# Kernel tuning notes

Hardware: AMD Instinct MI355X
Metric: run time of the kernel (lower is better)

## Reference

```python
import jax, jax.numpy as jnp
import numpy as np

N_A = 100000   # articles
N_U = 100000   # users
E   = 1600000  # edges per edge type (avg degree 16)
D_A = 300      # article text-embedding dim
D_U = 64       # user feature dim
H   = 64       # hidden_channels
OUT = 2        # out_channels


def _lin(k, out_d, in_d, scale=0.05):
    kw, kb = jax.random.split(k)
    return (jax.random.normal(kw, (out_d, in_d)) * scale,
            jax.random.normal(kb, (out_d,)) * scale)


def setup_inputs():
    key = jax.random.key(0)
    ks = jax.random.split(key, 20)
    inp = {
        "x_article": jax.random.normal(ks[0], (N_A, D_A)),
        "x_user":    jax.random.normal(ks[1], (N_U, D_U)),
        "ei_posts":  jax.random.randint(ks[2], (2, E), 0, N_U),  # user -> article (row0 src user, row1 dst article)
        "ei_pb":     jax.random.randint(ks[3], (2, E), 0, N_A),  # article -> user
    }
    # input projections per node type
    inp["w_in_a"], inp["b_in_a"] = _lin(ks[4], H, D_A)
    inp["w_in_u"], inp["b_in_u"] = _lin(ks[5], H, D_U)
    # SAGEConv params per (layer, edge type): lin_l (with bias) on aggregated src, lin_r (no bias) on dst
    i = 6
    for layer in ("c1", "c2"):
        for et in ("p", "b"):  # p = posts (user->article), b = posted_by (article->user)
            wl, bl = _lin(ks[i], H, H); i += 1
            wr, _  = _lin(ks[i], H, H); i += 1
            inp[f"{layer}{et}_wl"] = wl
            inp[f"{layer}{et}_bl"] = bl
            inp[f"{layer}{et}_wr"] = wr
    inp["w_out"], inp["b_out"] = _lin(ks[i], OUT, H)
    return inp


def _sage(x_src, x_dst, edge_index, wl, bl, wr, n_dst):
    """PyG SAGEConv((-1,-1), H): lin_l(mean_neighbors(x_src)) + lin_r(x_dst)."""
    src, dst = edge_index[0], edge_index[1]
    msg = x_src[src]                                        # [E, H] gather
    agg = jax.ops.segment_sum(msg, dst, num_segments=n_dst)  # [n_dst, H]
    cnt = jax.ops.segment_sum(jnp.ones((edge_index.shape[1],), x_src.dtype), dst, num_segments=n_dst)
    agg = agg / jnp.maximum(cnt, 1.0)[:, None]               # mean aggregation
    return agg @ wl.T + bl + x_dst @ wr.T


def reference(x_article, x_user, ei_posts, ei_pb,
              w_in_a, b_in_a, w_in_u, b_in_u,
              c1p_wl, c1p_bl, c1p_wr, c1b_wl, c1b_bl, c1b_wr,
              c2p_wl, c2p_bl, c2p_wr, c2b_wl, c2b_bl, c2b_wr,
              w_out, b_out):
    # per-node-type input projection + ReLU
    a = jax.nn.relu(x_article @ w_in_a.T + b_in_a)  # [N_A, H]
    u = jax.nn.relu(x_user @ w_in_u.T + b_in_u)      # [N_U, H]
    # conv1 (HeteroConv mean over edge types is trivial: 1 edge type per dst type) + ReLU
    a1 = jax.nn.relu(_sage(u, a, ei_posts, c1p_wl, c1p_bl, c1p_wr, N_A))
    u1 = jax.nn.relu(_sage(a, u, ei_pb,    c1b_wl, c1b_bl, c1b_wr, N_U))
    # conv2; only the 'article' output is used by the model head
    a2 = _sage(u1, a1, ei_posts, c2p_wl, c2p_bl, c2p_wr, N_A)
    return a2 @ w_out.T + b_out  # [N_A, OUT]
```

## Files before the change

kernel.cpp:

```cpp
#include <hip/hip_runtime.h>

#define N_NODES 100000
#define EDGES   1600000
#define H 64
#define OFFPAD 100352
#define NB2 391
#define CHUNK 8192
#define NCHUNK 196
#define LOSTRIDE 392

typedef unsigned int u32;
typedef unsigned short u16;
typedef short bf16x8 __attribute__((ext_vector_type(8)));
typedef float f32x4  __attribute__((ext_vector_type(4)));

__device__ __forceinline__ void bfsplit(float x, u32& h, u32& lo) {
    union { float f; u32 u; } c; c.f = x;
    u32 hu = (c.u + 0x7fffu + ((c.u >> 16) & 1u)) & 0xffff0000u;
    h = hu >> 16;
    union { u32 u; float f; } hb; hb.u = hu;
    union { float f; u32 u; } r; r.f = x - hb.f;
    lo = (r.u + 0x7fffu + ((r.u >> 16) & 1u)) >> 16;
}
__device__ __forceinline__ u16 bfrne(float x) {
    union { float f; u32 u; } c; c.f = x;
    return (u16)((c.u + 0x7fffu + ((c.u >> 16) & 1u)) >> 16);
}
__device__ __forceinline__ float bflo(u32 w)  { union { u32 u; float f; } c; c.u = w << 16; return c.f; }
__device__ __forceinline__ float bfhi(u32 w)  { union { u32 u; float f; } c; c.u = w & 0xffff0000u; return c.f; }

__global__ __launch_bounds__(256) void prep_weights(
    const float* __restrict__ w_a, const float* __restrict__ w_u,
    const float* __restrict__ b_wl, const float* __restrict__ b_wr,
    const float* __restrict__ p_wl, const float* __restrict__ p_wr,
    u32* __restrict__ pa_h, u32* __restrict__ pa_l,
    u32* __restrict__ pu_h, u32* __restrict__ pu_l,
    u32* __restrict__ pb_h, u32* __restrict__ pb_l,
    u32* __restrict__ pp_h, u32* __restrict__ pp_l)
{
    const int t = blockIdx.x * 256 + threadIdx.x;
    float v0 = 0.f, v1 = 0.f; u32* dh; u32* dl; int idx;
    if (t < 10240) {
        const int row = t / 160, u = t - row * 160, k = 2 * u;
        if (k < 300)     v0 = w_a[row * 300 + k];
        if (k + 1 < 300) v1 = w_a[row * 300 + k + 1];
        dh = pa_h; dl = pa_l; idx = t;
    } else if (t < 12288) {
        idx = t - 10240;
        const int row = idx >> 5, u = idx & 31, k = 2 * u;
        v0 = w_u[row * 64 + k]; v1 = w_u[row * 64 + k + 1];
        dh = pu_h; dl = pu_l;
    } else if (t < 16384) {
        idx = t - 12288;
        const int row = idx >> 6, u = idx & 63, k = 2 * u;
        if (k < 64) { v0 = b_wl[row * 64 + k];      v1 = b_wl[row * 64 + k + 1]; }
        else        { v0 = b_wr[row * 64 + k - 64]; v1 = b_wr[row * 64 + k - 63]; }
        dh = pb_h; dl = pb_l;
    } else {
        idx = t - 16384;
        const int row = idx >> 6, u = idx & 63, k = 2 * u;
        if (k < 64) { v0 = p_wl[row * 64 + k];      v1 = p_wl[row * 64 + k + 1]; }
        else        { v0 = p_wr[row * 64 + k - 64]; v1 = p_wr[row * 64 + k - 63]; }
        dh = pp_h; dl = pp_l;
    }
    u32 h0, l0, h1, l1; bfsplit(v0, h0, l0); bfsplit(v1, h1, l1);
    dh[idx] = h0 | (h1 << 16);
    dl[idx] = l0 | (l1 << 16);
}

template<int D, int KPAD>
__global__ __launch_bounds__(256) void proj_mfma(
    const float* __restrict__ x,
    const u32* __restrict__ wh_g, const u32* __restrict__ wl_g,
    const float* __restrict__ b, float* __restrict__ out, u16* __restrict__ outb)
{
    constexpr int NT = KPAD / 64;
    __shared__ u32 Xh[64 * 32], Xl[64 * 32], Wh[64 * 32], Wl[64 * 32];
    const int tid  = threadIdx.x;
    const int base = blockIdx.x * 64;
    const int l  = tid & 63;
    const int wv = tid >> 6;
    const int arow = wv * 16 + (l & 15);
    const int kg = l >> 4;
    f32x4 acc[4] = {};

    for (int t = 0; t < NT; ++t) {
        const int k0 = t * 64;
        for (int i = tid; i < 1024; i += 256) {
            const int row = i >> 4, j = i & 15;
            const int k = k0 + 4 * j;
            const int u = 2 * j;
            const int widx = (row << 5) | (u ^ ((row & 7) << 2));
            const int rr = min(base + row, N_NODES - 1);
            float4 v = make_float4(0.f, 0.f, 0.f, 0.f);
            if (k + 4 <= D) {
                v = *(const float4*)&x[(size_t)rr * D + k];
            } else {
                const float* xr = &x[(size_t)rr * D];
                if (k     < D) v.x = xr[k];
                if (k + 1 < D) v.y = xr[k + 1];
                if (k + 2 < D) v.z = xr[k + 2];
                if (k + 3 < D) v.w = xr[k + 3];
            }
            u32 h0, l0, h1, l1, h2, l2, h3, l3;
            bfsplit(v.x, h0, l0); bfsplit(v.y, h1, l1);
            bfsplit(v.z, h2, l2); bfsplit(v.w, h3, l3);
            *(uint2*)&Xh[widx] = make_uint2(h0 | (h1 << 16), h2 | (h3 << 16));
            *(uint2*)&Xl[widx] = make_uint2(l0 | (l1 << 16), l2 | (l3 << 16));
            const int wo = row * (KPAD / 2) + (k0 >> 1) + u;
            *(uint2*)&Wh[widx] = *(const uint2*)&wh_g[wo];
            *(uint2*)&Wl[widx] = *(const uint2*)&wl_g[wo];
        }
        __syncthreads();
        #pragma unroll
        for (int s = 0; s < 2; ++s) {
            const int ka = (arow << 5) + ((s * 16 + kg * 4) ^ ((arow & 7) << 2));
            const bf16x8 ah = *(const bf16x8*)&Xh[ka];
            const bf16x8 al = *(const bf16x8*)&Xl[ka];
            #pragma unroll
            for (int c = 0; c < 4; ++c) {
                const int brow = c * 16 + (l & 15);
                const int kb = (brow << 5) + ((s * 16 + kg * 4) ^ ((brow & 7) << 2));
                const bf16x8 bh = *(const bf16x8*)&Wh[kb];
                const bf16x8 bl = *(const bf16x8*)&Wl[kb];
                acc[c] = __builtin_amdgcn_mfma_f32_16x16x32_bf16(ah, bh, acc[c], 0, 0, 0);
                acc[c] = __builtin_amdgcn_mfma_f32_16x16x32_bf16(ah, bl, acc[c], 0, 0, 0);
                acc[c] = __builtin_amdgcn_mfma_f32_16x16x32_bf16(al, bh, acc[c], 0, 0, 0);
            }
        }
        __syncthreads();
    }

    const int orow0 = base + wv * 16 + (l >> 4) * 4;
    #pragma unroll
    for (int c = 0; c < 4; ++c) {
        const int col = c * 16 + (l & 15);
        const float bv = b[col];
        #pragma unroll
        for (int i = 0; i < 4; ++i) {
            const int row = orow0 + i;
            if (row < N_NODES) {
                const float v = fmaxf(acc[c][i] + bv, 0.f);
                out[(size_t)row * H + col] = v;
                outb[(size_t)row * H + col] = bfrne(v);
            }
        }
    }
}

__global__ __launch_bounds__(256) void sort_fill(
    const int* __restrict__ ei_p, const int* __restrict__ ei_b,
    int* __restrict__ lo_p, int* __restrict__ lo_b,
    int* __restrict__ sz_p, int* __restrict__ sz_b,
    int* __restrict__ raw_p, int* __restrict__ raw_b)
{
    __shared__ int cnt[NB2];
    __shared__ int loc[NB2 + 1];
    int b = blockIdx.x;
    const int* __restrict__ ei; int* __restrict__ lo; int* __restrict__ sz; int* __restrict__ raw;
    if (b < NCHUNK) { ei = ei_p; lo = lo_p; sz = sz_p; raw = raw_p; }
    else { b -= NCHUNK; ei = ei_b; lo = lo_b; sz = sz_b; raw = raw_b; }
    const int tid = threadIdx.x;
    const int e0 = b * CHUNK, e1 = min(e0 + CHUNK, EDGES);

    for (int i = tid; i < NB2; i += 256) cnt[i] = 0;
    __syncthreads();
    for (int e = e0 + tid; e < e1; e += 256)
        atomicAdd(&cnt[ei[EDGES + e] >> 8], 1);
    __syncthreads();
    for (int i = tid; i < NB2; i += 256)
        if (cnt[i]) atomicAdd(&sz[i], cnt[i]);
    if (tid == 0) {
        int run = 0;
        for (int i = 0; i < NB2; ++i) { loc[i] = run; run += cnt[i]; }
        loc[NB2] = run;
    }
    __syncthreads();
    for (int i = tid; i <= NB2; i += 256) lo[b * LOSTRIDE + i] = loc[i];
    for (int i = tid; i < NB2; i += 256) cnt[i] = loc[i];
    __syncthreads();
    for (int e = e0 + tid; e < e1; e += 256) {
        const int d = ei[EDGES + e], s = ei[e];
        const int pos = atomicAdd(&cnt[d >> 8], 1);
        raw[e0 + pos] = (s << 8) | (d & 255);
    }
}

__global__ __launch_bounds__(256) void scan_boff(
    const int* __restrict__ sz_p, const int* __restrict__ sz_b,
    int* __restrict__ boff_p, int* __restrict__ boff_b,
    int* __restrict__ off_p, int* __restrict__ off_b)
{
    __shared__ int part[256];
    const int* sz = blockIdx.x ? sz_b : sz_p;
    int* boff = blockIdx.x ? boff_b : boff_p;
    int* off  = blockIdx.x ? off_b : off_p;
    const int t = threadIdx.x;
    const int i0 = 2 * t, i1 = 2 * t + 1;
    const int v0 = (i0 < NB2) ? sz[i0] : 0;
    const int v1 = (i1 < NB2) ? sz[i1] : 0;
    part[t] = v0 + v1;
    __syncthreads();
    for (int d = 1; d < 256; d <<= 1) {
        int x = (t >= d) ? part[t - d] : 0;
        __syncthreads();
        part[t] += x;
        __syncthreads();
    }
    const int excl = part[t] - (v0 + v1);
    if (i0 < NB2) boff[i0] = excl;
    if (i1 < NB2) boff[i1] = excl + v0;
    if (t == 0) { boff[NB2] = EDGES; off[N_NODES] = EDGES; }
}

__global__ __launch_bounds__(256) void bucket_sort2(
    const int* __restrict__ raw_p, const int* __restrict__ raw_b,
    const int* __restrict__ lo_p, const int* __restrict__ lo_b,
    const int* __restrict__ boff_p, const int* __restrict__ boff_b,
    int* __restrict__ off_p, int* __restrict__ off_b,
    int* __restrict__ csr_p, int* __restrict__ csr_b)
{
    __shared__ int cnt[256];
    __shared__ int cur[256];
    __shared__ int sb[NCHUNK], se[NCHUNK];
    int k = blockIdx.x;
    const int* raw; const int* lo; const int* boff; int* off; int* csr;
    if (k < NB2) { raw = raw_p; lo = lo_p; boff = boff_p; off = off_p; csr = csr_p; }
    else { k -= NB2; raw = raw_b; lo = lo_b; boff = boff_b; off = off_b; csr = csr_b; }
    const int tid = threadIdx.x;
    cnt[tid] = 0;
    if (tid < NCHUNK) {
        sb[tid] = lo[tid * LOSTRIDE + k];
        se[tid] = lo[tid * LOSTRIDE + k + 1];
    }
    __syncthreads();
    if (tid < NCHUNK) {
        const int base = tid * CHUNK;
        for (int e = sb[tid]; e < se[tid]; ++e)
            atomicAdd(&cnt[raw[base + e] & 255], 1);
    }
    __syncthreads();
    if (tid == 0) {
        int run = boff[k];
        for (int i = 0; i < 256; ++i) { cur[i] = run; run += cnt[i]; }
    }
    __syncthreads();
    {
        const int node = (k << 8) + tid;
        if (node < N_NODES) off[node] = cur[tid];
    }
    __syncthreads();
    if (tid < NCHUNK) {
        const int base = tid * CHUNK;
        for (int e = sb[tid]; e < se[tid]; ++e) {
            const int id = raw[base + e];
            const int pos = atomicAdd(&cur[id & 255], 1);
            csr[pos] = id >> 8;
        }
    }
}

__global__ __launch_bounds__(256) void gather_bf16(
    const u16* __restrict__ featb, const int* __restrict__ off,
    const int* __restrict__ csr, float* __restrict__ agg)
{
    const int node = (blockIdx.x * 256 + threadIdx.x) >> 6;
    const int lane = threadIdx.x & 63;
    const int grp  = lane >> 3;
    const int q    = lane & 7;
    const u32* fb = (const u32*)featb;
    const int beg = off[node], end = off[node + 1];
    float a0=0.f,a1=0.f,a2=0.f,a3=0.f,a4=0.f,a5=0.f,a6=0.f,a7=0.f;
    for (int e = beg + grp; e < end; e += 8) {
        const int s = csr[e];
        const uint4 v = *(const uint4*)&fb[((size_t)s << 5) + (q << 2)];
        a0 += bflo(v.x); a1 += bfhi(v.x);
        a2 += bflo(v.y); a3 += bfhi(v.y);
        a4 += bflo(v.z); a5 += bfhi(v.z);
        a6 += bflo(v.w); a7 += bfhi(v.w);
    }
    #pragma unroll
    for (int m = 8; m <= 32; m <<= 1) {
        a0 += __shfl_xor(a0, m, 64); a1 += __shfl_xor(a1, m, 64);
        a2 += __shfl_xor(a2, m, 64); a3 += __shfl_xor(a3, m, 64);
        a4 += __shfl_xor(a4, m, 64); a5 += __shfl_xor(a5, m, 64);
        a6 += __shfl_xor(a6, m, 64); a7 += __shfl_xor(a7, m, 64);
    }
    if (grp == 0) {
        const float inv = 1.0f / fmaxf((float)(end - beg), 1.0f);
        float4 o0 = make_float4(a0 * inv, a1 * inv, a2 * inv, a3 * inv);
        float4 o1 = make_float4(a4 * inv, a5 * inv, a6 * inv, a7 * inv);
        *(float4*)&agg[(size_t)node * H + 8 * q]     = o0;
        *(float4*)&agg[(size_t)node * H + 8 * q + 4] = o1;
    }
}

__global__ __launch_bounds__(256) void fold_head(
    const float* __restrict__ w_out, const float* __restrict__ wl2,
    const float* __restrict__ wr2, const float* __restrict__ bl2,
    const float* __restrict__ b_out, float* __restrict__ headW)
{
    const int t = threadIdx.x;
    if (t < 128) {
        int o = t >> 6, j = t & 63;
        float s = 0.f;
        for (int h = 0; h < 64; ++h) s += w_out[o * 64 + h] * wl2[h * 64 + j];
        headW[o * 64 + j] = s;
    } else {
        int idx = t - 128, o = idx >> 6, j = idx & 63;
        float s = 0.f;
        for (int h = 0; h < 64; ++h) s += w_out[o * 64 + h] * wr2[h * 64 + j];
        headW[128 + o * 64 + j] = s;
    }
    if (t < 2) {
        float s = b_out[t];
        for (int h = 0; h < 64; ++h) s += w_out[t * 64 + h] * bl2[h];
        headW[256 + t] = s;
    }
}

template<bool ZHEAD>
__global__ __launch_bounds__(256) void sage_mfma(
    const float* __restrict__ A1, const float* __restrict__ A2,
    const u32* __restrict__ wh_g, const u32* __restrict__ wl_g,
    const float* __restrict__ bias,
    const float* __restrict__ headW, float* __restrict__ z,
    float* __restrict__ outA)
{
    __shared__ u32 Ah[4096], Al[4096];
    union ShW { u32 w[4096]; float us[64 * 65]; };
    __shared__ ShW shw;
    const int tid  = threadIdx.x;
    const int base = blockIdx.x * 64;
    const int l  = tid & 63;
    const int wv = tid >> 6;
    const int arow = wv * 16 + (l & 15);
    const int kg = l >> 4;
    f32x4 acc[4] = {};

    for (int i = tid; i < 4096; i += 256) {
        const int row = i >> 6, u = i & 63;
        const int k = 2 * u;
        const int rr = min(base + row, N_NODES - 1);
        const float2 v = (k < 64)
            ? *(const float2*)&A1[(size_t)rr * H + k]
            : *(const float2*)&A2[(size_t)rr * H + (k - 64)];
        u32 h0, l0, h1, l1;
        bfsplit(v.x, h0, l0); bfsplit(v.y, h1, l1);
        const int widx = (row << 6) | (u ^ ((row & 7) << 2));
        Ah[widx] = h0 | (h1 << 16);
        Al[widx] = l0 | (l1 << 16);
    }

    #pragma unroll
    for (int t = 0; t < 2; ++t) {
        for (int i = tid; i < 2048; i += 256) {
            const int row = i >> 5, u = i & 31;
            const int widx = (row << 5) | (u ^ ((row & 7) << 2));
            shw.w[widx]        = wh_g[row * 64 + t * 32 + u];
            shw.w[2048 + widx] = wl_g[row * 64 + t * 32 + u];
        }
        __syncthreads();
        #pragma unroll
        for (int s = 0; s < 2; ++s) {
            const int ka = (arow << 6) + ((t * 32 + s * 16 + kg * 4) ^ ((arow & 7) << 2));
            const bf16x8 ah = *(const bf16x8*)&Ah[ka];
            const bf16x8 al = *(const bf16x8*)&Al[ka];
            #pragma unroll
            for (int c = 0; c < 4; ++c) {
                const int brow = c * 16 + (l & 15);
                const int kb = (brow << 5) + ((s * 16 + kg * 4) ^ ((brow & 7) << 2));
                const bf16x8 bh = *(const bf16x8*)&shw.w[kb];
                const bf16x8 bl = *(const bf16x8*)&shw.w[2048 + kb];
                acc[c] = __builtin_amdgcn_mfma_f32_16x16x32_bf16(ah, bh, acc[c], 0, 0, 0);
                acc[c] = __builtin_amdgcn_mfma_f32_16x16x32_bf16(ah, bl, acc[c], 0, 0, 0);
                acc[c] = __builtin_amdgcn_mfma_f32_16x16x32_bf16(al, bh, acc[c], 0, 0, 0);
            }
        }
        __syncthreads();
    }

    const int r0 = wv * 16 + (l >> 4) * 4;
    if (!ZHEAD) {
        #pragma unroll
        for (int c = 0; c < 4; ++c) {
            const int col = c * 16 + (l & 15);
            const float bv = bias[col];
            #pragma unroll
            for (int i = 0; i < 4; ++i) {
                const int row = base + r0 + i;
                if (row < N_NODES)
                    outA[(size_t)row * H + col] = fmaxf(acc[c][i] + bv, 0.f);
            }
        }
    } else {
        #pragma unroll
        for (int c = 0; c < 4; ++c) {
            const int col = c * 16 + (l & 15);
            const float bv = bias[col];
            #pragma unroll
            for (int i = 0; i < 4; ++i)
                shw.us[(r0 + i) * 65 + col] = fmaxf(acc[c][i] + bv, 0.f);
        }
        __syncthreads();
        if (tid < 128) {
            const int r = tid & 63, o = tid >> 6;
            const int row = base + r;
            if (row < N_NODES) {
                float v = 0.f;
                for (int k = 0; k < 64; ++k)
                    v += shw.us[r * 65 + k] * headW[o * 64 + k];
                z[(size_t)row * 2 + o] = v;
            }
        }
    }
}

__global__ __launch_bounds__(256) void final_head(
    const int* __restrict__ off, const int* __restrict__ csr,
    const float* __restrict__ z, const float* __restrict__ a1,
    const float* __restrict__ headW, float* __restrict__ out)
{
    const int node = (blockIdx.x * 256 + threadIdx.x) >> 6;
    const int lane = threadIdx.x & 63;
    const int beg = off[node], end = off[node + 1];
    float z0 = 0.f, z1 = 0.f;
    for (int e = beg + lane; e < end; e += 64) {
        int s = csr[e];
        const float2 zv = *(const float2*)&z[(size_t)s * 2];
        z0 += zv.x; z1 += zv.y;
    }
    const float av = a1[(size_t)node * H + lane];
    float p0 = av * headW[128 + lane];
    float p1 = av * headW[192 + lane];
    #pragma unroll
    for (int m = 1; m <= 32; m <<= 1) {
        z0 += __shfl_xor(z0, m, 64);
        z1 += __shfl_xor(z1, m, 64);
        p0 += __shfl_xor(p0, m, 64);
        p1 += __shfl_xor(p1, m, 64);
    }
    if (lane == 0) {
        const float inv = 1.0f / fmaxf((float)(end - beg), 1.0f);
        float2 o;
        o.x = z0 * inv + p0 + headW[256];
        o.y = z1 * inv + p1 + headW[257];
        *(float2*)&out[(size_t)node * 2] = o;
    }
}

extern "C" void kernel_launch(void* const* d_in, const int* in_sizes, int n_in,
                              void* d_out, int out_size, void* d_ws, size_t ws_size,
                              hipStream_t stream) {
    const float* x_a    = (const float*)d_in[0];
    const float* x_u    = (const float*)d_in[1];
    const int*   ei_p   = (const int*)d_in[2];
    const int*   ei_b   = (const int*)d_in[3];
    const float* w_in_a = (const float*)d_in[4];
    const float* b_in_a = (const float*)d_in[5];
    const float* w_in_u = (const float*)d_in[6];
    const float* b_in_u = (const float*)d_in[7];
    const float* c1p_wl = (const float*)d_in[8];
    const float* c1p_bl = (const float*)d_in[9];
    const float* c1p_wr = (const float*)d_in[10];
    const float* c1b_wl = (const float*)d_in[11];
    const float* c1b_bl = (const float*)d_in[12];
    const float* c1b_wr = (const float*)d_in[13];
    const float* c2p_wl = (const float*)d_in[14];
    const float* c2p_bl = (const float*)d_in[15];
    const float* c2p_wr = (const float*)d_in[16];
    const float* w_out  = (const float*)d_in[20];
    const float* b_out  = (const float*)d_in[21];

    const size_t NF = (size_t)N_NODES * H;
    float* bufA  = (float*)d_ws;
    float* bufU  = bufA + NF;
    float* agg   = bufU + NF;
    u16*   fAb   = (u16*)(agg + NF);
    u16*   fUb   = fAb + NF;
    float* z     = (float*)(fUb + NF);
    float* headW = z + 2 * N_NODES;
    int* lo_p   = (int*)(headW + 512);
    int* lo_b   = lo_p + 77056;
    int* sz_p   = lo_b + 77056;
    int* sz_b   = sz_p + 512;
    int* boff_p = sz_b + 512;
    int* boff_b = boff_p + 512;
    int* off_p  = boff_b + 512;
    int* off_b  = off_p + OFFPAD;
    int* csr_p  = off_b + OFFPAD;
    int* csr_b  = csr_p + EDGES;
    u32* pa_h   = (u32*)(csr_b + EDGES);
    u32* pa_l   = pa_h + 10240;
    u32* pu_h   = pa_l + 10240;
    u32* pu_l   = pu_h + 2048;
    u32* pb_h   = pu_l + 2048;
    u32* pb_l   = pb_h + 4096;
    u32* pp_h   = pb_l + 4096;
    u32* pp_l   = pp_h + 4096;
    int* raw_p  = (int*)agg;
    int* raw_b  = raw_p + EDGES;

    const dim3 blk(256);
    const int grid_gemm = (N_NODES + 63) / 64;

    prep_weights<<<80, blk, 0, stream>>>(
        w_in_a, w_in_u, c1b_wl, c1b_wr, c1p_wl, c1p_wr,
        pa_h, pa_l, pu_h, pu_l, pb_h, pb_l, pp_h, pp_l);
    fold_head<<<1, blk, 0, stream>>>(w_out, c2p_wl, c2p_wr, c2p_bl, b_out, headW);

    hipMemsetAsync(sz_p, 0, 2 * 512 * sizeof(int), stream);
    sort_fill<<<2 * NCHUNK, blk, 0, stream>>>(
        ei_p, ei_b, lo_p, lo_b, sz_p, sz_b, raw_p, raw_b);
    scan_boff<<<2, blk, 0, stream>>>(sz_p, sz_b, boff_p, boff_b, off_p, off_b);
    bucket_sort2<<<2 * NB2, blk, 0, stream>>>(
        raw_p, raw_b, lo_p, lo_b, boff_p, boff_b, off_p, off_b, csr_p, csr_b);

    proj_mfma<300, 320><<<grid_gemm, blk, 0, stream>>>(x_a, pa_h, pa_l, b_in_a, bufA, fAb);
    proj_mfma<64, 64>  <<<grid_gemm, blk, 0, stream>>>(x_u, pu_h, pu_l, b_in_u, bufU, fUb);

    gather_bf16<<<25000, blk, 0, stream>>>(fAb, off_b, csr_b, agg);
    sage_mfma<true><<<grid_gemm, blk, 0, stream>>>(
        agg, bufU, pb_h, pb_l, c1b_bl, headW, z, nullptr);

    gather_bf16<<<25000, blk, 0, stream>>>(fUb, off_p, csr_p, agg);
    sage_mfma<false><<<grid_gemm, blk, 0, stream>>>(
        agg, bufA, pp_h, pp_l, c1p_bl, headW, nullptr, bufA);

    final_head<<<25000, blk, 0, stream>>>(off_p, csr_p, z, bufA, headW, (float*)d_out);

    (void)in_sizes; (void)n_in; (void)out_size; (void)ws_size;
}
```

Before: 396.3 us.

## Enlarge projection GEMM tile to 128 rows and prefetch next X tile into registers

The input projection kernel now handles 128 rows per block, so each wave computes two 16-row groups and the weight tile staged in shared memory is reused across more rows. It also software-pipelines the K loop: the next X slice is loaded from global memory into registers while the current slice is consumed by MFMA. This targets the memory-bound x_article projection, which streams about 120 MB. In exchange it uses more registers and shared memory per block and launches half as many blocks, which may reduce occupancy.

```diff
diff --git a/kernel.cpp b/kernel.cpp
--- a/kernel.cpp
+++ b/kernel.cpp
@@ -68,29 +68,31 @@
     dl[idx] = l0 | (l1 << 16);
 }
 
-template<int D, int KPAD>
+template<int D, int KPAD, int ROWS>
 __global__ __launch_bounds__(256) void proj_mfma(
     const float* __restrict__ x,
     const u32* __restrict__ wh_g, const u32* __restrict__ wl_g,
     const float* __restrict__ b, float* __restrict__ out, u16* __restrict__ outb)
 {
     constexpr int NT = KPAD / 64;
-    __shared__ u32 Xh[64 * 32], Xl[64 * 32], Wh[64 * 32], Wl[64 * 32];
+    constexpr int PER_THR = (ROWS * 16) / 256;
+    constexpr int NG = ROWS / 64;
+    __shared__ u32 Xh[ROWS * 32], Xl[ROWS * 32], Wh[64 * 32], Wl[64 * 32];
     const int tid  = threadIdx.x;
-    const int base = blockIdx.x * 64;
+    const int base = blockIdx.x * ROWS;
     const int l  = tid & 63;
     const int wv = tid >> 6;
-    const int arow = wv * 16 + (l & 15);
     const int kg = l >> 4;
-    f32x4 acc[4] = {};
-
-    for (int t = 0; t < NT; ++t) {
+    f32x4 acc[NG][4] = {};
+
+    float4 xreg[PER_THR];
+    auto loadX = [&](int t) {
         const int k0 = t * 64;
-        for (int i = tid; i < 1024; i += 256) {
+        #pragma unroll
+        for (int it = 0; it < PER_THR; ++it) {
+            const int i = tid + it * 256;
             const int row = i >> 4, j = i & 15;
             const int k = k0 + 4 * j;
-            const int u = 2 * j;
-            const int widx = (row << 5) | (u ^ ((row & 7) << 2));
             const int rr = min(base + row, N_NODES - 1);
             float4 v = make_float4(0.f, 0.f, 0.f, 0.f);
             if (k + 4 <= D) {
@@ -102,47 +104,77 @@
                 if (k + 2 < D) v.z = xr[k + 2];
                 if (k + 3 < D) v.w = xr[k + 3];
             }
+            xreg[it] = v;
+        }
+    };
+
+    loadX(0);
+    for (int t = 0; t < NT; ++t) {
+        #pragma unroll
+        for (int it = 0; it < PER_THR; ++it) {
+            const int i = tid + it * 256;
+            const int row = i >> 4, j = i & 15;
+            const int u = 2 * j;
+            const int widx = (row << 5) | (u ^ ((row & 7) << 2));
             u32 h0, l0, h1, l1, h2, l2, h3, l3;
-            bfsplit(v.x, h0, l0); bfsplit(v.y, h1, l1);
-            bfsplit(v.z, h2, l2); bfsplit(v.w, h3, l3);
+            bfsplit(xreg[it].x, h0, l0); bfsplit(xreg[it].y, h1, l1);
+            bfsplit(xreg[it].z, h2, l2); bfsplit(xreg[it].w, h3, l3);
             *(uint2*)&Xh[widx] = make_uint2(h0 | (h1 << 16), h2 | (h3 << 16));
             *(uint2*)&Xl[widx] = make_uint2(l0 | (l1 << 16), l2 | (l3 << 16));
-            const int wo = row * (KPAD / 2) + (k0 >> 1) + u;
-            *(uint2*)&Wh[widx] = *(const uint2*)&wh_g[wo];
-            *(uint2*)&Wl[widx] = *(const uint2*)&wl_g[wo];
-        }
+        }
+        {
+            const int k0 = t * 64;
+            #pragma unroll
+            for (int it = 0; it < 4; ++it) {
+                const int i = tid + it * 256;
+                const int row = i >> 4, j = i & 15;
+                const int u = 2 * j;
+                const int widx = (row << 5) | (u ^ ((row & 7) << 2));
+                const int wo = row * (KPAD / 2) + (k0 >> 1) + u;
+                *(uint2*)&Wh[widx] = *(const uint2*)&wh_g[wo];
+                *(uint2*)&Wl[widx] = *(const uint2*)&wl_g[wo];
+            }
+        }
+        if (t + 1 < NT) loadX(t + 1);
         __syncthreads();
         #pragma unroll
         for (int s = 0; s < 2; ++s) {
-            const int ka = (arow << 5) + ((s * 16 + kg * 4) ^ ((arow & 7) << 2));
-            const bf16x8 ah = *(const bf16x8*)&Xh[ka];
-            const bf16x8 al = *(const bf16x8*)&Xl[ka];
             #pragma unroll
-            for (int c = 0; c < 4; ++c) {
-                const int brow = c * 16 + (l & 15);
-                const int kb = (brow << 5) + ((s * 16 + kg * 4) ^ ((brow & 7) << 2));
-                const bf16x8 bh = *(const bf16x8*)&Wh[kb];
-                const bf16x8 bl = *(const bf16x8*)&Wl[kb];
-                acc[c] = __builtin_amdgcn_mfma_f32_16x16x32_bf16(ah, bh, acc[c], 0, 0, 0);
-                acc[c] = __builtin_amdgcn_mfma_f32_16x16x32_bf16(ah, bl, acc[c], 0, 0, 0);
-                acc[c] = __builtin_amdgcn_mfma_f32_16x16x32_bf16(al, bh, acc[c], 0, 0, 0);
-            }
-        }
-        __syncthreads();
-    }
-
-    const int orow0 = base + wv * 16 + (l >> 4) * 4;
+            for (int g = 0; g < NG; ++g) {
+                const int arow = wv * (NG * 16) + g * 16 + (l & 15);
+                const int ka = (arow << 5) + ((s * 16 + kg * 4) ^ ((arow & 7) << 2));
+                const bf16x8 ah = *(const bf16x8*)&Xh[ka];
+                const bf16x8 al = *(const bf16x8*)&Xl[ka];
+                #pragma unroll
+                for (int c = 0; c < 4; ++c) {
+                    const int brow = c * 16 + (l & 15);
+                    const int kb = (brow << 5) + ((s * 16 + kg * 4) ^ ((brow & 7) << 2));
+                    const bf16x8 bh = *(const bf16x8*)&Wh[kb];
+                    const bf16x8 bl = *(const bf16x8*)&Wl[kb];
+                    acc[g][c] = __builtin_amdgcn_mfma_f32_16x16x32_bf16(ah, bh, acc[g][c], 0, 0, 0);
+                    acc[g][c] = __builtin_amdgcn_mfma_f32_16x16x32_bf16(ah, bl, acc[g][c], 0, 0, 0);
+                    acc[g][c] = __builtin_amdgcn_mfma_f32_16x16x32_bf16(al, bh, acc[g][c], 0, 0, 0);
+                }
+            }
+        }
+        __syncthreads();
+    }
+
     #pragma unroll
-    for (int c = 0; c < 4; ++c) {
-        const int col = c * 16 + (l & 15);
-        const float bv = b[col];
-        #pragma unroll
-        for (int i = 0; i < 4; ++i) {
-            const int row = orow0 + i;
-            if (row < N_NODES) {
-                const float v = fmaxf(acc[c][i] + bv, 0.f);
-                out[(size_t)row * H + col] = v;
-                outb[(size_t)row * H + col] = bfrne(v);
+    for (int g = 0; g < NG; ++g) {
+        const int orow0 = base + wv * (NG * 16) + g * 16 + (l >> 4) * 4;
+        #pragma unroll
+        for (int c = 0; c < 4; ++c) {
+            const int col = c * 16 + (l & 15);
+            const float bv = b[col];
+            #pragma unroll
+            for (int i = 0; i < 4; ++i) {
+                const int row = orow0 + i;
+                if (row < N_NODES) {
+                    const float v = fmaxf(acc[g][c][i] + bv, 0.f);
+                    out[(size_t)row * H + col] = v;
+                    outb[(size_t)row * H + col] = bfrne(v);
+                }
             }
         }
     }
@@ -503,6 +535,7 @@
 
     const dim3 blk(256);
     const int grid_gemm = (N_NODES + 63) / 64;
+    const int grid_proj = (N_NODES + 127) / 128;
 
     prep_weights<<<80, blk, 0, stream>>>(
         w_in_a, w_in_u, c1b_wl, c1b_wr, c1p_wl, c1p_wr,
@@ -516,8 +549,8 @@
     bucket_sort2<<<2 * NB2, blk, 0, stream>>>(
         raw_p, raw_b, lo_p, lo_b, boff_p, boff_b, off_p, off_b, csr_p, csr_b);
 
-    proj_mfma<300, 320><<<grid_gemm, blk, 0, stream>>>(x_a, pa_h, pa_l, b_in_a, bufA, fAb);
-    proj_mfma<64, 64>  <<<grid_gemm, blk, 0, stream>>>(x_u, pu_h, pu_l, b_in_u, bufU, fUb);
+    proj_mfma<300, 320, 128><<<grid_proj, blk, 0, stream>>>(x_a, pa_h, pa_l, b_in_a, bufA, fAb);
+    proj_mfma<64, 64, 128>  <<<grid_proj, blk, 0, stream>>>(x_u, pu_h, pu_l, b_in_u, bufU, fUb);
 
     gather_bf16<<<25000, blk, 0, stream>>>(fAb, off_b, csr_b, agg);
     sage_mfma<true><<<grid_gemm, blk, 0, stream>>>(
```

After: 405.7 us. 2.4% more time.
